# Kernel optimization log

Measured on AMD Instinct MI355X. Metric: run time of the kernel, lower is better.

The kernel has to match this reference:

```python
import jax, jax.numpy as jnp
import numpy as np

D_MODEL = 1024
N_HEADS = 16
D_HEAD = D_MODEL // N_HEADS
D_FF = 4 * D_MODEL
EPS = 1e-5


def _layernorm(x, g, b):
    mu = jnp.mean(x, axis=-1, keepdims=True)
    var = jnp.var(x, axis=-1, keepdims=True)
    return (x - mu) * jax.lax.rsqrt(var + EPS) * g + b


def setup_inputs() -> dict:
    key = jax.random.key(0)
    ks = jax.random.split(key, 16)
    s_attn = 1.0 / np.sqrt(D_MODEL)
    s_ff1 = 1.0 / np.sqrt(D_MODEL)
    s_ff2 = 1.0 / np.sqrt(D_FF)
    inp = {
        'x': jax.random.normal(ks[0], (2, 2048, D_MODEL), dtype=jnp.float32),
        'Wq': jax.random.uniform(ks[1], (D_MODEL, D_MODEL), jnp.float32, -s_attn, s_attn),
        'bq': jax.random.uniform(ks[2], (D_MODEL,), jnp.float32, -s_attn, s_attn),
        'Wk': jax.random.uniform(ks[3], (D_MODEL, D_MODEL), jnp.float32, -s_attn, s_attn),
        'bk': jax.random.uniform(ks[4], (D_MODEL,), jnp.float32, -s_attn, s_attn),
        'Wv': jax.random.uniform(ks[5], (D_MODEL, D_MODEL), jnp.float32, -s_attn, s_attn),
        'bv': jax.random.uniform(ks[6], (D_MODEL,), jnp.float32, -s_attn, s_attn),
        'Wo': jax.random.uniform(ks[7], (D_MODEL, D_MODEL), jnp.float32, -s_attn, s_attn),
        'bo': jax.random.uniform(ks[8], (D_MODEL,), jnp.float32, -s_attn, s_attn),
        'W1': jax.random.uniform(ks[9], (D_MODEL, D_FF), jnp.float32, -s_ff1, s_ff1),
        'b1': jax.random.uniform(ks[10], (D_FF,), jnp.float32, -s_ff1, s_ff1),
        'W2': jax.random.uniform(ks[11], (D_FF, D_MODEL), jnp.float32, -s_ff2, s_ff2),
        'b2': jax.random.uniform(ks[12], (D_MODEL,), jnp.float32, -s_ff2, s_ff2),
        'ln1_g': jnp.ones((D_MODEL,), jnp.float32),
        'ln1_b': jnp.zeros((D_MODEL,), jnp.float32),
        'ln2_g': jnp.ones((D_MODEL,), jnp.float32),
        'ln2_b': jnp.zeros((D_MODEL,), jnp.float32),
    }
    return inp


def reference(x, Wq, bq, Wk, bk, Wv, bv, Wo, bo, W1, b1, W2, b2, ln1_g, ln1_b, ln2_g, ln2_b):
    B, T, D = x.shape
    scale = D_HEAD ** -0.5

    # pre-norm MHSA + residual
    h = _layernorm(x, ln1_g, ln1_b)
    def split(z):  # [B,T,D] -> [B,H,T,d_h]
        return z.reshape(B, T, N_HEADS, D_HEAD).transpose(0, 2, 1, 3)
    Q = split(h @ Wq + bq)
    K = split(h @ Wk + bk)
    V = split(h @ Wv + bv)
    scores = jnp.einsum('bhqd,bhkd->bhqk', Q, K) * scale  # [B,H,T,T]
    attn = jax.nn.softmax(scores, axis=-1)
    out = jnp.einsum('bhqk,bhkd->bhqd', attn, V)
    out = out.transpose(0, 2, 1, 3).reshape(B, T, D)
    x = x + (out @ Wo + bo)

    # pre-norm FFN + residual
    h = _layernorm(x, ln2_g, ln2_b)
    ff = jax.nn.gelu(h @ W1 + b1, approximate=False) @ W2 + b2
    return x + ff
```

## Files before the change

kernel.cpp:

```cpp
#include <hip/hip_runtime.h>
#include <math.h>

#define SEQ   2048
#define DM    1024
#define LDQKV 3072
#define MTOK  4096

typedef float  f32x4   __attribute__((ext_vector_type(4)));
typedef __bf16 bf16x8  __attribute__((ext_vector_type(8)));
typedef short  short8  __attribute__((ext_vector_type(8)));
typedef short  short4v __attribute__((ext_vector_type(4)));

__device__ __forceinline__ short f2bf(float f) {
  union { float f; unsigned u; } v; v.f = f;
  unsigned r = v.u + 0x7fffu + ((v.u >> 16) & 1u);
  return (short)(r >> 16);
}

__device__ __forceinline__ void gl_lds16(const void* g, void* l) {
  __builtin_amdgcn_global_load_lds(
      (const __attribute__((address_space(1))) void*)g,
      (__attribute__((address_space(3))) void*)l, 16, 0, 0);
}

__device__ __forceinline__ f32x4 mfma_bf16(bf16x8 a, bf16x8 b, f32x4 c) {
  return __builtin_amdgcn_mfma_f32_16x16x32_bf16(a, b, c, 0, 0, 0);
}

__device__ __forceinline__ float gelu_f(float x) {
  const float z  = x * 0.70710678118654752f;
  const float az = fabsf(z);
  const float t  = __builtin_amdgcn_rcpf(fmaf(0.3275911f, az, 1.0f));
  float p = fmaf(1.061405429f, t, -1.453152027f);
  p = fmaf(p, t, 1.421413741f);
  p = fmaf(p, t, -0.284496736f);
  p = fmaf(p, t, 0.254829592f);
  p = p * t;
  const float e = __builtin_amdgcn_exp2f(az * az * -1.4426950408889634f);
  float erfp = fmaf(-p, e, 1.0f);
  erfp = (z < 0.f) ? -erfp : erfp;
  return x * fmaf(0.5f, erfp, 0.5f);
}

__global__ __launch_bounds__(256) void transpose_all_k(
    const float* __restrict__ Wq, const float* __restrict__ Wk,
    const float* __restrict__ Wv, const float* __restrict__ Wo,
    const float* __restrict__ W1, const float* __restrict__ W2,
    short* __restrict__ Wqt, short* __restrict__ Wkt, short* __restrict__ Wvt,
    short* __restrict__ Wot, short* __restrict__ W1t, short* __restrict__ W2t)
{
  const int bid = blockIdx.x;
  const float* W; short* Wt; int K, N, nx, ky;
  if (bid < 1024) {
    const int m = bid >> 8, r = bid & 255;
    W  = (m == 0) ? Wq : (m == 1) ? Wk : (m == 2) ? Wv : Wo;
    Wt = (m == 0) ? Wqt : (m == 1) ? Wkt : (m == 2) ? Wvt : Wot;
    K = 1024; N = 1024; nx = r & 15; ky = r >> 4;
  } else if (bid < 2048) {
    const int r = bid - 1024;
    W = W1; Wt = W1t; K = 1024; N = 4096; nx = r & 63; ky = r >> 6;
  } else {
    const int r = bid - 2048;
    W = W2; Wt = W2t; K = 4096; N = 1024; nx = r & 15; ky = r >> 4;
  }
  const int n0 = nx * 64, k0 = ky * 64;

  __shared__ float tile[64][65];
  const int tid = threadIdx.x;
  const int lr = tid >> 4, lc = (tid & 15) * 4;
#pragma unroll
  for (int i = 0; i < 4; i++) {
    const float4 v = *(const float4*)&W[(size_t)(k0 + lr + i * 16) * N + n0 + lc];
    tile[lr + i * 16][lc]     = v.x;
    tile[lr + i * 16][lc + 1] = v.y;
    tile[lr + i * 16][lc + 2] = v.z;
    tile[lr + i * 16][lc + 3] = v.w;
  }
  __syncthreads();
  const int nr = tid >> 3, ks = (tid & 7) * 8;
#pragma unroll
  for (int i = 0; i < 2; i++) {
    short8 o;
#pragma unroll
    for (int j = 0; j < 8; j++) o[j] = f2bf(tile[ks + j][nr + i * 32]);
    *(short8*)&Wt[(size_t)(n0 + nr + i * 32) * K + k0 + ks] = o;
  }
}

__global__ __launch_bounds__(256) void ln_k(
    const float* __restrict__ x, const float* __restrict__ g,
    const float* __restrict__ b, short* __restrict__ out)
{
  const int row = blockIdx.x;
  const int tid = threadIdx.x;
  const float4 v = ((const float4*)(x + (size_t)row * DM))[tid];
  float s  = v.x + v.y + v.z + v.w;
  float ss = v.x * v.x + v.y * v.y + v.z * v.z + v.w * v.w;
#pragma unroll
  for (int m = 32; m >= 1; m >>= 1) { s += __shfl_xor(s, m); ss += __shfl_xor(ss, m); }
  __shared__ float red[8];
  const int wid = tid >> 6;
  if ((tid & 63) == 0) { red[wid] = s; red[4 + wid] = ss; }
  __syncthreads();
  s  = red[0] + red[1] + red[2] + red[3];
  ss = red[4] + red[5] + red[6] + red[7];
  const float mu  = s * (1.f / DM);
  const float var = ss * (1.f / DM) - mu * mu;
  const float rs  = rsqrtf(var + 1e-5f);
  const float4 gv = ((const float4*)g)[tid];
  const float4 bv = ((const float4*)b)[tid];
  short4v o;
  o[0] = f2bf((v.x - mu) * rs * gv.x + bv.x);
  o[1] = f2bf((v.y - mu) * rs * gv.y + bv.y);
  o[2] = f2bf((v.z - mu) * rs * gv.z + bv.z);
  o[3] = f2bf((v.w - mu) * rs * gv.w + bv.w);
  *(short4v*)(out + (size_t)row * DM + tid * 4) = o;
}

__global__ __launch_bounds__(256) void concat_bias_k(
    const float* __restrict__ bq, const float* __restrict__ bk,
    const float* __restrict__ bv, float* __restrict__ o)
{
  int i = blockIdx.x * 256 + threadIdx.x;
  if (i < 3072) {
    float v = (i < 1024) ? bq[i] : (i < 2048 ? bk[i - 1024] : bv[i - 2048]);
    o[i] = v;
  }
}

__global__ __launch_bounds__(256) void vtrans_k(
    const short* __restrict__ V, short* __restrict__ Vt)
{
  const int b = blockIdx.z, h = blockIdx.y, t0 = blockIdx.x * 64;
  __shared__ short tile[64][72];
  const int tid = threadIdx.x;
  const int r = tid >> 2, c = (tid & 3) * 16;
  const short* src = V + (size_t)(b * SEQ + t0 + r) * LDQKV + h * 64 + c;
  *(short8*)&tile[r][c]     = *(const short8*)src;
  *(short8*)&tile[r][c + 8] = *(const short8*)(src + 8);
  __syncthreads();
  const int d = tid >> 2;
  short8 o0, o1;
#pragma unroll
  for (int k = 0; k < 8; k++) o0[k] = tile[c + k][d];
#pragma unroll
  for (int k = 0; k < 8; k++) o1[k] = tile[c + 8 + k][d];
  short* dst = Vt + (((size_t)(b * 16 + h) * 64) + d) * 2048 + t0 + c;
  *(short8*)dst       = o0;
  *(short8*)(dst + 8) = o1;
}

template <bool GELU_, bool RESID, bool OUTBF16>
__global__ __launch_bounds__(512) void gemm256(
    const short* __restrict__ A, const short* __restrict__ Bt,
    const float* __restrict__ bias, const float* __restrict__ resid,
    void* __restrict__ Cout, int M, int N, int K)
{
  __shared__ __align__(16) short Atile[2][256 * 64];
  __shared__ __align__(16) short Btile[2][256 * 64];

  const int tid = threadIdx.x, lane = tid & 63, wid = tid >> 6;
  const int wm = wid >> 2, wn = wid & 3;

  const int nbn = N >> 8;
  const int chunk = gridDim.x >> 3;
  const int swz = (blockIdx.x & 7) * chunk + (blockIdx.x >> 3);
  const int bm = (swz / nbn) * 256;
  const int bn = (swz % nbn) * 256;

  f32x4 acc[8][4] = {};

  const int srow  = wid * 8 + (lane >> 3);
  const int sslot = (lane & 7) ^ ((lane >> 3) & 7);
  const short* Asrc = A  + (size_t)(bm + srow) * K + sslot * 8;
  const short* Bsrc = Bt + (size_t)(bn + srow) * K + sslot * 8;

#define STAGE256(buf, k0)                                                     \
  {                                                                           \
    _Pragma("unroll")                                                         \
    for (int j = 0; j < 4; j++) {                                             \
      gl_lds16(Asrc + (size_t)(j * 64) * K + (k0), &Atile[buf][(j * 64 + wid * 8) * 64]); \
      gl_lds16(Bsrc + (size_t)(j * 64) * K + (k0), &Btile[buf][(j * 64 + wid * 8) * 64]); \
    }                                                                         \
  }

  const int aRowBase = (wm * 128 + (lane & 15)) * 128;
  const int bRowBase = (wn * 64  + (lane & 15)) * 128;
  const int slot0 = (((lane >> 4)    ) ^ (lane & 7)) * 16;
  const int slot1 = (((lane >> 4) + 4) ^ (lane & 7)) * 16;

#define COMPUTE256(buf)                                                       \
  {                                                                           \
    const char* Ab_ = (const char*)&Atile[buf][0];                            \
    const char* Bb_ = (const char*)&Btile[buf][0];                            \
    _Pragma("unroll")                                                         \
    for (int ks = 0; ks < 2; ks++) {                                          \
      const int sl = ks ? slot1 : slot0;                                      \
      bf16x8 a[8], b[4];                                                      \
      _Pragma("unroll")                                                       \
      for (int mi = 0; mi < 8; mi++)                                          \
        a[mi] = *(const bf16x8*)(Ab_ + aRowBase + mi * 2048 + sl);            \
      _Pragma("unroll")                                                       \
      for (int ni = 0; ni < 4; ni++)                                          \
        b[ni] = *(const bf16x8*)(Bb_ + bRowBase + ni * 2048 + sl);            \
      __builtin_amdgcn_s_setprio(1);                                          \
      _Pragma("unroll")                                                       \
      for (int mi = 0; mi < 8; mi++)                                          \
        _Pragma("unroll")                                                     \
        for (int ni = 0; ni < 4; ni++)                                        \
          acc[mi][ni] = mfma_bf16(a[mi], b[ni], acc[mi][ni]);                 \
      __builtin_amdgcn_s_setprio(0);                                          \
    }                                                                         \
  }

  STAGE256(0, 0);
  __syncthreads();

  int cur = 0;
  const int ntiles = K >> 6;
  for (int t = 1; t < ntiles; ++t) {
    STAGE256(cur ^ 1, t * 64);
    COMPUTE256(cur);
    __syncthreads();
    cur ^= 1;
  }
  COMPUTE256(cur);

#pragma unroll
  for (int mi = 0; mi < 8; mi++) {
#pragma unroll
    for (int ni = 0; ni < 4; ni++) {
      const int col = bn + wn * 64 + ni * 16 + (lane & 15);
      const float bs = bias[col];
#pragma unroll
      for (int j = 0; j < 4; j++) {
        const int row = bm + wm * 128 + mi * 16 + (lane >> 4) * 4 + j;
        float v = acc[mi][ni][j] + bs;
        if (GELU_) v = gelu_f(v);
        if (RESID) v += resid[(size_t)row * N + col];
        if (OUTBF16) ((short*)Cout)[(size_t)row * N + col] = f2bf(v);
        else         ((float*)Cout)[(size_t)row * N + col] = v;
      }
    }
  }
#undef STAGE256
#undef COMPUTE256
}

template <bool GELU_, bool RESID, bool OUTBF16>
__global__ __launch_bounds__(512) void gemm256d3(
    const short* __restrict__ A, const short* __restrict__ Bt,
    const float* __restrict__ bias, const float* __restrict__ resid,
    void* __restrict__ Cout, int M, int N, int K)
{
  __shared__ __align__(16) short Ash[4][256 * 32];
  __shared__ __align__(16) short Bsh[4][256 * 32];

  const int tid = threadIdx.x, lane = tid & 63, wid = tid >> 6;
  const int wm = wid >> 2, wn = wid & 3;

  const int nbn = N >> 8;
  const int chunk = gridDim.x >> 3;
  const int swz = (blockIdx.x & 7) * chunk + (blockIdx.x >> 3);
  const int bm = (swz / nbn) * 256;
  const int bn = (swz % nbn) * 256;

  f32x4 acc[8][4] = {};

  const int srow = tid >> 2;
  const int scol = ((tid & 3) ^ ((srow >> 1) & 3)) * 8;
  const short* Asrc = A  + (size_t)(bm + srow) * K + scol;
  const short* Bsrc = Bt + (size_t)(bn + srow) * K + scol;
  const int d0 = (wid * 16) * 32, d1 = (128 + wid * 16) * 32;

#define STAGE_D3(buf, k0)                                                     \
  {                                                                           \
    gl_lds16(Asrc + (k0),                   &Ash[buf][d0]);                   \
    gl_lds16(Asrc + (size_t)128 * K + (k0), &Ash[buf][d1]);                   \
    gl_lds16(Bsrc + (k0),                   &Bsh[buf][d0]);                   \
    gl_lds16(Bsrc + (size_t)128 * K + (k0), &Bsh[buf][d1]);                   \
  }

  const int rslot = ((lane >> 4) ^ ((lane >> 1) & 3)) * 8;
  const int aOff  = (wm * 128 + (lane & 15)) * 32 + rslot;
  const int bOff  = (wn * 64  + (lane & 15)) * 32 + rslot;

#define COMPUTE_D3(buf)                                                       \
  {                                                                           \
    const short* Ab_ = &Ash[buf][0];                                          \
    const short* Bb_ = &Bsh[buf][0];                                          \
    bf16x8 a[8], b[4];                                                        \
    _Pragma("unroll")                                                         \
    for (int mi = 0; mi < 8; mi++)                                            \
      a[mi] = *(const bf16x8*)(Ab_ + aOff + mi * 512);                        \
    _Pragma("unroll")                                                         \
    for (int ni = 0; ni < 4; ni++)                                            \
      b[ni] = *(const bf16x8*)(Bb_ + bOff + ni * 512);                        \
    __builtin_amdgcn_s_setprio(1);                                            \
    _Pragma("unroll")                                                         \
    for (int mi = 0; mi < 8; mi++)                                            \
      _Pragma("unroll")                                                       \
      for (int ni = 0; ni < 4; ni++)                                          \
        acc[mi][ni] = mfma_bf16(a[mi], b[ni], acc[mi][ni]);                   \
    __builtin_amdgcn_s_setprio(0);                                            \
  }

  const int nt = K >> 5;

  STAGE_D3(0, 0);
  STAGE_D3(1, 32);
  STAGE_D3(2, 64);
  asm volatile("s_waitcnt vmcnt(8)" ::: "memory");
  __builtin_amdgcn_s_barrier();
  __builtin_amdgcn_sched_barrier(0);

  for (int t = 0; t < nt; ++t) {
    if (t + 3 < nt) STAGE_D3((t + 3) & 3, (t + 3) * 32);
    COMPUTE_D3(t & 3);
    if (t + 3 < nt)      { asm volatile("s_waitcnt vmcnt(8)" ::: "memory"); }
    else if (t + 2 < nt) { asm volatile("s_waitcnt vmcnt(4)" ::: "memory"); }
    else if (t + 1 < nt) { asm volatile("s_waitcnt vmcnt(0)" ::: "memory"); }
    __builtin_amdgcn_s_barrier();
    __builtin_amdgcn_sched_barrier(0);
  }

#pragma unroll
  for (int mi = 0; mi < 8; mi++) {
#pragma unroll
    for (int ni = 0; ni < 4; ni++) {
      const int col = bn + wn * 64 + ni * 16 + (lane & 15);
      const float bs = bias[col];
#pragma unroll
      for (int j = 0; j < 4; j++) {
        const int row = bm + wm * 128 + mi * 16 + (lane >> 4) * 4 + j;
        float v = acc[mi][ni][j] + bs;
        if (GELU_) v = gelu_f(v);
        if (RESID) v += resid[(size_t)row * N + col];
        if (OUTBF16) ((short*)Cout)[(size_t)row * N + col] = f2bf(v);
        else         ((float*)Cout)[(size_t)row * N + col] = v;
      }
    }
  }
#undef STAGE_D3
#undef COMPUTE_D3
}

template <bool GELU_, bool RESID, bool OUTBF16>
__global__ __launch_bounds__(512) void gemm_bt8(
    const short* __restrict__ A, const short* __restrict__ Bt,
    const float* __restrict__ bias, const float* __restrict__ resid,
    void* __restrict__ Cout, int M, int N, int K)
{
  __shared__ __align__(16) short Ab[2][2][128 * 32];
  __shared__ __align__(16) short Bb[2][2][64 * 32];
  const int tid = threadIdx.x, lane = tid & 63, wid = tid >> 6;
  const int kg = wid >> 2, w2 = wid & 3;
  const int wr = w2 >> 1, wc = w2 & 1;
  const int bm = blockIdx.x * 128, bn = blockIdx.y * 64;

  f32x4 acc[4][2] = {};

  const int r_l = lane >> 2;
  const int c8  = ((lane & 3) ^ ((lane >> 3) & 3)) * 8;
  const short* Ag0 = A  + (size_t)(bm + w2 * 32 + r_l)      * K + c8;
  const short* Ag1 = A  + (size_t)(bm + w2 * 32 + 16 + r_l) * K + c8;
  const short* Bg0 = Bt + (size_t)(bn + w2 * 16 + r_l)      * K + c8;

  const int la0 = (w2 * 32) * 32, la1 = (w2 * 32 + 16) * 32, lb0 = (w2 * 16) * 32;
  const int kbase = kg * 32;
  const int rslot = ((lane >> 4) ^ ((lane >> 1) & 3)) * 8;

  gl_lds16(Ag0 + kbase, &Ab[kg][0][la0]);
  gl_lds16(Ag1 + kbase, &Ab[kg][0][la1]);
  gl_lds16(Bg0 + kbase, &Bb[kg][0][lb0]);
  __syncthreads();

  const int nsteps = K >> 6;
  int cur = 0;
  for (int i = 1; i < nsteps; ++i) {
    const int k0 = i * 64 + kbase;
    const int nxt = cur ^ 1;
    gl_lds16(Ag0 + k0, &Ab[kg][nxt][la0]);
    gl_lds16(Ag1 + k0, &Ab[kg][nxt][la1]);
    gl_lds16(Bg0 + k0, &Bb[kg][nxt][lb0]);

    bf16x8 a[4], b[2];
#pragma unroll
    for (int mi = 0; mi < 4; mi++)
      a[mi] = *(const bf16x8*)&Ab[kg][cur][(wr * 64 + mi * 16 + (lane & 15)) * 32 + rslot];
#pragma unroll
    for (int ni = 0; ni < 2; ni++)
      b[ni] = *(const bf16x8*)&Bb[kg][cur][(wc * 32 + ni * 16 + (lane & 15)) * 32 + rslot];
#pragma unroll
    for (int mi = 0; mi < 4; mi++)
#pragma unroll
      for (int ni = 0; ni < 2; ni++)
        acc[mi][ni] = mfma_bf16(a[mi], b[ni], acc[mi][ni]);

    __syncthreads();
    cur = nxt;
  }

  {
    bf16x8 a[4], b[2];
#pragma unroll
    for (int mi = 0; mi < 4; mi++)
      a[mi] = *(const bf16x8*)&Ab[kg][cur][(wr * 64 + mi * 16 + (lane & 15)) * 32 + rslot];
#pragma unroll
    for (int ni = 0; ni < 2; ni++)
      b[ni] = *(const bf16x8*)&Bb[kg][cur][(wc * 32 + ni * 16 + (lane & 15)) * 32 + rslot];
#pragma unroll
    for (int mi = 0; mi < 4; mi++)
#pragma unroll
      for (int ni = 0; ni < 2; ni++)
        acc[mi][ni] = mfma_bf16(a[mi], b[ni], acc[mi][ni]);
  }

  __syncthreads();

  float* red = (float*)&Ab[0][0][0];
  const int lslot = w2 * 64 + lane;
  if (kg == 1) {
    *(f32x4*)&red[((0 * 256) + lslot) * 4]        = acc[0][0];
    *(f32x4*)&red[((1 * 256) + lslot) * 4]        = acc[0][1];
    *(f32x4*)&red[((2 * 256) + lslot) * 4]        = acc[1][0];
    *(f32x4*)&red[((3 * 256) + lslot) * 4]        = acc[1][1];
  } else {
    *(f32x4*)&red[((1024 + 0 * 256) + lslot) * 4] = acc[2][0];
    *(f32x4*)&red[((1024 + 1 * 256) + lslot) * 4] = acc[2][1];
    *(f32x4*)&red[((1024 + 2 * 256) + lslot) * 4] = acc[3][0];
    *(f32x4*)&red[((1024 + 3 * 256) + lslot) * 4] = acc[3][1];
  }
  __syncthreads();

#define BT8_STORE(MI, NI)                                                     \
  {                                                                           \
    const int col = bn + wc * 32 + (NI) * 16 + (lane & 15);                   \
    const float bs = bias[col];                                               \
    _Pragma("unroll")                                                         \
    for (int j = 0; j < 4; j++) {                                             \
      const int row = bm + wr * 64 + (MI) * 16 + (lane >> 4) * 4 + j;         \
      float v = acc[MI][NI][j] + bs;                                          \
      if (GELU_) v = gelu_f(v);                                               \
      if (RESID) v += resid[(size_t)row * N + col];                           \
      if (OUTBF16) ((short*)Cout)[(size_t)row * N + col] = f2bf(v);           \
      else         ((float*)Cout)[(size_t)row * N + col] = v;                 \
    }                                                                         \
  }

  if (kg == 0) {
    acc[0][0] += *(const f32x4*)&red[((0 * 256) + lslot) * 4];
    acc[0][1] += *(const f32x4*)&red[((1 * 256) + lslot) * 4];
    acc[1][0] += *(const f32x4*)&red[((2 * 256) + lslot) * 4];
    acc[1][1] += *(const f32x4*)&red[((3 * 256) + lslot) * 4];
    BT8_STORE(0, 0); BT8_STORE(0, 1); BT8_STORE(1, 0); BT8_STORE(1, 1);
  } else {
    acc[2][0] += *(const f32x4*)&red[((1024 + 0 * 256) + lslot) * 4];
    acc[2][1] += *(const f32x4*)&red[((1024 + 1 * 256) + lslot) * 4];
    acc[3][0] += *(const f32x4*)&red[((1024 + 2 * 256) + lslot) * 4];
    acc[3][1] += *(const f32x4*)&red[((1024 + 3 * 256) + lslot) * 4];
    BT8_STORE(2, 0); BT8_STORE(2, 1); BT8_STORE(3, 0); BT8_STORE(3, 1);
  }
#undef BT8_STORE
}

__global__ __launch_bounds__(512, 4) void attn_k(
    const short* __restrict__ Qg, const short* __restrict__ Kg,
    const short* __restrict__ Vt, short* __restrict__ Og)
{
  const int phys = blockIdx.x;
  const int lg = (phys & 7) * 64 + (phys >> 3);
  const int q0 = (lg & 15) * 128;
  const int h  = (lg >> 4) & 15;
  const int b  = lg >> 8;

  const int tid = threadIdx.x, lane = tid & 63, w = tid >> 6;
  const int qlane = lane & 15, g = lane >> 4;

  __shared__ __align__(16) short Kl[2][128 * 64];
  __shared__ __align__(16) short Vl[2][64 * 128];

  const size_t qrow = (size_t)(b * SEQ + q0 + w * 16 + qlane) * LDQKV + h * 64;
  const bf16x8 qf0 = *(const bf16x8*)&Qg[qrow + g * 8];
  const bf16x8 qf1 = *(const bf16x8*)&Qg[qrow + 32 + g * 8];

  const int kslot = (lane & 7) ^ ((lane >> 3) & 7);
  const short* Kg_a[2];
#pragma unroll
  for (int i = 0; i < 2; i++) {
    const int r  = i * 64 + w * 8 + (lane >> 3);
    const int kc = r >> 4, gr = (r >> 2) & 3, jr = r & 3;
    const int a  = 32 * (kc & 3) + 8 * gr + 4 * (kc >> 2) + jr;
    Kg_a[i] = Kg + ((size_t)(b * SEQ) + a) * LDQKV + h * 64 + kslot * 8;
  }
  const short* Vg_s[2];
#pragma unroll
  for (int i = 0; i < 2; i++) {
    const int d  = i * 32 + w * 4 + (lane >> 4);
    const int vs = (lane & 15) ^ (d & 15);
    Vg_s[i] = Vt + ((size_t)(b * 16 + h) * 64 + d) * 2048 + vs * 8;
  }

  float m_run = -1e30f, l_run = 0.f;
  f32x4 oacc[4] = {};
  const float C = 0.125f * 1.44269504088896f;

#pragma unroll
  for (int i = 0; i < 2; i++) {
    gl_lds16(Kg_a[i], &Kl[0][(i * 64 + w * 8) * 64]);
    gl_lds16(Vg_s[i], &Vl[0][(i * 32 + w * 4) * 128]);
  }
  __syncthreads();

  int cur = 0;
  for (int kt = 0; kt < SEQ; kt += 128) {
    const int nxt = cur ^ 1;
    if (kt + 128 < SEQ) {
#pragma unroll
      for (int i = 0; i < 2; i++) {
        gl_lds16(Kg_a[i] + (size_t)(kt + 128) * LDQKV, &Kl[nxt][(i * 64 + w * 8) * 64]);
        gl_lds16(Vg_s[i] + (kt + 128),                 &Vl[nxt][(i * 32 + w * 4) * 128]);
      }
    }
    const char* KbC = (const char*)&Kl[cur][0];
    const char* VbC = (const char*)&Vl[cur][0];

    f32x4 s[8];
#pragma unroll
    for (int kc = 0; kc < 8; kc++) {
      const int kr = kc * 16 + qlane;
      const char* kp = KbC + kr * 128;
      const int sw = (kr & 7) << 4;
      bf16x8 kf0 = *(const bf16x8*)(kp + ((g * 16) ^ sw));
      bf16x8 kf1 = *(const bf16x8*)(kp + ((64 + g * 16) ^ sw));
      f32x4 z = {};
      z = mfma_bf16(kf0, qf0, z);
      z = mfma_bf16(kf1, qf1, z);
      s[kc] = z;
    }

    f32x4 m4 = s[0];
#pragma unroll
    for (int kc = 1; kc < 8; kc++) {
      m4[0] = fmaxf(m4[0], s[kc][0]); m4[1] = fmaxf(m4[1], s[kc][1]);
      m4[2] = fmaxf(m4[2], s[kc][2]); m4[3] = fmaxf(m4[3], s[kc][3]);
    }
    float mt = fmaxf(fmaxf(m4[0], m4[1]), fmaxf(m4[2], m4[3]));
    mt = fmaxf(mt, __shfl_xor(mt, 16));
    mt = fmaxf(mt, __shfl_xor(mt, 32));

    if (!__all(mt - m_run <= 40.0f)) {
      const float mnew = fmaxf(m_run, mt);
      const float r = __builtin_amdgcn_exp2f((m_run - mnew) * C);
      m_run = mnew;
      l_run *= r;
#pragma unroll
      for (int j = 0; j < 4; j++) {
        const float rj = __shfl(r, g * 4 + j);
#pragma unroll
        for (int dt = 0; dt < 4; dt++) oacc[dt][j] *= rj;
      }
    }

    const float nmc = -m_run * C;
    float rs = 0.f;
    unsigned pw[4][4];
#pragma unroll
    for (int kc = 0; kc < 8; kc++) {
      f32x4 p;
#pragma unroll
      for (int j = 0; j < 4; j++) p[j] = __builtin_amdgcn_exp2f(fmaf(s[kc][j], C, nmc));
      rs += (p[0] + p[1]) + (p[2] + p[3]);
      unsigned w0, w1;
      asm("v_cvt_pk_bf16_f32 %0, %1, %2" : "=v"(w0) : "v"(p[0]), "v"(p[1]));
      asm("v_cvt_pk_bf16_f32 %0, %1, %2" : "=v"(w1) : "v"(p[2]), "v"(p[3]));
      pw[kc & 3][2 * (kc >> 2) + 0] = w0;
      pw[kc & 3][2 * (kc >> 2) + 1] = w1;
    }
    rs += __shfl_xor(rs, 16);
    rs += __shfl_xor(rs, 32);
    l_run += rs;

#pragma unroll
    for (int ks = 0; ks < 4; ks++) {
      union { unsigned u[4]; bf16x8 v; } pf;
      pf.u[0] = pw[ks][0]; pf.u[1] = pw[ks][1];
      pf.u[2] = pw[ks][2]; pf.u[3] = pw[ks][3];
#pragma unroll
      for (int dt = 0; dt < 4; dt++) {
        const int vr = dt * 16 + qlane;
        bf16x8 vf = *(const bf16x8*)(VbC + vr * 256 + ((64 * ks + 16 * g) ^ ((vr & 15) << 4)));
        oacc[dt] = mfma_bf16(pf.v, vf, oacc[dt]);
      }
    }

    __syncthreads();
    cur = nxt;
  }

  const float linv = 1.f / l_run;
#pragma unroll
  for (int j = 0; j < 4; j++) {
    const float lj = __shfl(linv, g * 4 + j);
    const int tok = q0 + w * 16 + g * 4 + j;
#pragma unroll
    for (int dt = 0; dt < 4; dt++)
      Og[(size_t)(b * SEQ + tok) * DM + h * 64 + dt * 16 + qlane] = f2bf(oacc[dt][j] * lj);
  }
}

extern "C" void kernel_launch(void* const* d_in, const int* in_sizes, int n_in,
                              void* d_out, int out_size, void* d_ws, size_t ws_size,
                              hipStream_t stream)
{
  const float* x    = (const float*)d_in[0];
  const float* Wq   = (const float*)d_in[1];
  const float* bq   = (const float*)d_in[2];
  const float* Wk   = (const float*)d_in[3];
  const float* bk   = (const float*)d_in[4];
  const float* Wv   = (const float*)d_in[5];
  const float* bv   = (const float*)d_in[6];
  const float* Wo   = (const float*)d_in[7];
  const float* bo   = (const float*)d_in[8];
  const float* W1   = (const float*)d_in[9];
  const float* b1   = (const float*)d_in[10];
  const float* W2   = (const float*)d_in[11];
  const float* b2   = (const float*)d_in[12];
  const float* ln1g = (const float*)d_in[13];
  const float* ln1b = (const float*)d_in[14];
  const float* ln2g = (const float*)d_in[15];
  const float* ln2b = (const float*)d_in[16];

  char* ws = (char*)d_ws;
  const size_t MB = 1024 * 1024;
  short* Wqkvt = (short*)(ws + 0 * MB);
  short* Wqt   = Wqkvt;
  short* Wkt   = (short*)(ws + 2 * MB);
  short* Wvt   = (short*)(ws + 4 * MB);
  short* Wot   = (short*)(ws + 6 * MB);
  short* W1t   = (short*)(ws + 8 * MB);
  short* W2t   = (short*)(ws + 16 * MB);
  short* hbuf  = (short*)(ws + 24 * MB);
  short* QKV   = (short*)(ws + 32 * MB);
  short* AO    = (short*)(ws + 56 * MB);
  float* x1    = (float*)(ws + 64 * MB);
  short* Vtb   = (short*)(ws + 64 * MB);
  float* bqkv  = (float*)(ws + 80 * MB);
  short* gbuf  = (short*)(ws + 32 * MB);

  dim3 tb(256);

  transpose_all_k<<<dim3(3072), tb, 0, stream>>>(
      Wq, Wk, Wv, Wo, W1, W2, Wqt, Wkt, Wvt, Wot, W1t, W2t);
  concat_bias_k<<<dim3(12), tb, 0, stream>>>(bq, bk, bv, bqkv);

  ln_k<<<dim3(MTOK), tb, 0, stream>>>(x, ln1g, ln1b, hbuf);

  gemm256<false, false, true><<<dim3(192), dim3(512), 0, stream>>>(
      hbuf, Wqkvt, bqkv, nullptr, QKV, MTOK, 3072, 1024);

  vtrans_k<<<dim3(32, 16, 2), tb, 0, stream>>>(QKV + 2048, Vtb);

  attn_k<<<dim3(512), dim3(512), 0, stream>>>(QKV, QKV + 1024, Vtb, AO);

  gemm_bt8<false, true, false><<<dim3(32, 16), dim3(512), 0, stream>>>(
      AO, Wot, bo, x, x1, MTOK, 1024, 1024);

  ln_k<<<dim3(MTOK), tb, 0, stream>>>(x1, ln2g, ln2b, hbuf);

  gemm256d3<true, false, true><<<dim3(256), dim3(512), 0, stream>>>(
      hbuf, W1t, b1, nullptr, gbuf, MTOK, 4096, 1024);

  gemm_bt8<false, true, false><<<dim3(32, 16), dim3(512), 0, stream>>>(
      gbuf, W2t, b2, x1, (float*)d_out, MTOK, 1024, 4096);
}
```

Baseline: 243.8 us.

## Replace split-K 128x64 GEMM with 128x128 tile, 4-stage LDS pipeline

```diff
diff --git a/kernel.cpp b/kernel.cpp
--- a/kernel.cpp
+++ b/kernel.cpp
@@ -346,122 +346,105 @@
 }
 
 template <bool GELU_, bool RESID, bool OUTBF16>
-__global__ __launch_bounds__(512) void gemm_bt8(
+__global__ __launch_bounds__(512) void gemm128d3(
     const short* __restrict__ A, const short* __restrict__ Bt,
     const float* __restrict__ bias, const float* __restrict__ resid,
     void* __restrict__ Cout, int M, int N, int K)
 {
-  __shared__ __align__(16) short Ab[2][2][128 * 32];
-  __shared__ __align__(16) short Bb[2][2][64 * 32];
+  __shared__ __align__(16) short Ash[4][128 * 64];
+  __shared__ __align__(16) short Bsh[4][128 * 64];
+
   const int tid = threadIdx.x, lane = tid & 63, wid = tid >> 6;
-  const int kg = wid >> 2, w2 = wid & 3;
-  const int wr = w2 >> 1, wc = w2 & 1;
-  const int bm = blockIdx.x * 128, bn = blockIdx.y * 64;
+  const int wm = wid >> 2, wn = wid & 3;
+
+  const int nbn = N >> 7;
+  const int chunk = gridDim.x >> 3;
+  const int swz = (blockIdx.x & 7) * chunk + (blockIdx.x >> 3);
+  const int bm = (swz / nbn) * 128;
+  const int bn = (swz % nbn) * 128;
 
   f32x4 acc[4][2] = {};
 
-  const int r_l = lane >> 2;
-  const int c8  = ((lane & 3) ^ ((lane >> 3) & 3)) * 8;
-  const short* Ag0 = A  + (size_t)(bm + w2 * 32 + r_l)      * K + c8;
-  const short* Ag1 = A  + (size_t)(bm + w2 * 32 + 16 + r_l) * K + c8;
-  const short* Bg0 = Bt + (size_t)(bn + w2 * 16 + r_l)      * K + c8;
-
-  const int la0 = (w2 * 32) * 32, la1 = (w2 * 32 + 16) * 32, lb0 = (w2 * 16) * 32;
-  const int kbase = kg * 32;
-  const int rslot = ((lane >> 4) ^ ((lane >> 1) & 3)) * 8;
-
-  gl_lds16(Ag0 + kbase, &Ab[kg][0][la0]);
-  gl_lds16(Ag1 + kbase, &Ab[kg][0][la1]);
-  gl_lds16(Bg0 + kbase, &Bb[kg][0][lb0]);
-  __syncthreads();
-
-  const int nsteps = K >> 6;
-  int cur = 0;
-  for (int i = 1; i < nsteps; ++i) {
-    const int k0 = i * 64 + kbase;
-    const int nxt = cur ^ 1;
-    gl_lds16(Ag0 + k0, &Ab[kg][nxt][la0]);
-    gl_lds16(Ag1 + k0, &Ab[kg][nxt][la1]);
-    gl_lds16(Bg0 + k0, &Bb[kg][nxt][lb0]);
-
-    bf16x8 a[4], b[2];
-#pragma unroll
-    for (int mi = 0; mi < 4; mi++)
-      a[mi] = *(const bf16x8*)&Ab[kg][cur][(wr * 64 + mi * 16 + (lane & 15)) * 32 + rslot];
-#pragma unroll
-    for (int ni = 0; ni < 2; ni++)
-      b[ni] = *(const bf16x8*)&Bb[kg][cur][(wc * 32 + ni * 16 + (lane & 15)) * 32 + rslot];
-#pragma unroll
-    for (int mi = 0; mi < 4; mi++)
-#pragma unroll
-      for (int ni = 0; ni < 2; ni++)
-        acc[mi][ni] = mfma_bf16(a[mi], b[ni], acc[mi][ni]);
-
-    __syncthreads();
-    cur = nxt;
-  }
-
-  {
-    bf16x8 a[4], b[2];
-#pragma unroll
-    for (int mi = 0; mi < 4; mi++)
-      a[mi] = *(const bf16x8*)&Ab[kg][cur][(wr * 64 + mi * 16 + (lane & 15)) * 32 + rslot];
-#pragma unroll
-    for (int ni = 0; ni < 2; ni++)
-      b[ni] = *(const bf16x8*)&Bb[kg][cur][(wc * 32 + ni * 16 + (lane & 15)) * 32 + rslot];
-#pragma unroll
-    for (int mi = 0; mi < 4; mi++)
-#pragma unroll
-      for (int ni = 0; ni < 2; ni++)
-        acc[mi][ni] = mfma_bf16(a[mi], b[ni], acc[mi][ni]);
-  }
-
-  __syncthreads();
-
-  float* red = (float*)&Ab[0][0][0];
-  const int lslot = w2 * 64 + lane;
-  if (kg == 1) {
-    *(f32x4*)&red[((0 * 256) + lslot) * 4]        = acc[0][0];
-    *(f32x4*)&red[((1 * 256) + lslot) * 4]        = acc[0][1];
-    *(f32x4*)&red[((2 * 256) + lslot) * 4]        = acc[1][0];
-    *(f32x4*)&red[((3 * 256) + lslot) * 4]        = acc[1][1];
-  } else {
-    *(f32x4*)&red[((1024 + 0 * 256) + lslot) * 4] = acc[2][0];
-    *(f32x4*)&red[((1024 + 1 * 256) + lslot) * 4] = acc[2][1];
-    *(f32x4*)&red[((1024 + 2 * 256) + lslot) * 4] = acc[3][0];
-    *(f32x4*)&red[((1024 + 3 * 256) + lslot) * 4] = acc[3][1];
-  }
-  __syncthreads();
-
-#define BT8_STORE(MI, NI)                                                     \
+  const int srow  = wid * 8 + (lane >> 3);
+  const int sslot = (lane & 7) ^ ((lane >> 3) & 7);
+  const short* Asrc = A  + (size_t)(bm + srow) * K + sslot * 8;
+  const short* Bsrc = Bt + (size_t)(bn + srow) * K + sslot * 8;
+
+#define STAGE_128(buf, k0)                                                    \
   {                                                                           \
-    const int col = bn + wc * 32 + (NI) * 16 + (lane & 15);                   \
-    const float bs = bias[col];                                               \
+    gl_lds16(Asrc + (k0),                  &Ash[buf][(wid * 8) * 64]);        \
+    gl_lds16(Asrc + (size_t)64 * K + (k0), &Ash[buf][(64 + wid * 8) * 64]);   \
+    gl_lds16(Bsrc + (k0),                  &Bsh[buf][(wid * 8) * 64]);        \
+    gl_lds16(Bsrc + (size_t)64 * K + (k0), &Bsh[buf][(64 + wid * 8) * 64]);   \
+  }
+
+  const int aRowBase = (wm * 64 + (lane & 15)) * 128;
+  const int bRowBase = (wn * 32 + (lane & 15)) * 128;
+  const int slot0 = (((lane >> 4)    ) ^ (lane & 7)) * 16;
+  const int slot1 = (((lane >> 4) + 4) ^ (lane & 7)) * 16;
+
+#define COMPUTE_128(buf)                                                      \
+  {                                                                           \
+    const char* Ab_ = (const char*)&Ash[buf][0];                              \
+    const char* Bb_ = (const char*)&Bsh[buf][0];                              \
     _Pragma("unroll")                                                         \
-    for (int j = 0; j < 4; j++) {                                             \
-      const int row = bm + wr * 64 + (MI) * 16 + (lane >> 4) * 4 + j;         \
-      float v = acc[MI][NI][j] + bs;                                          \
-      if (GELU_) v = gelu_f(v);                                               \
-      if (RESID) v += resid[(size_t)row * N + col];                           \
-      if (OUTBF16) ((short*)Cout)[(size_t)row * N + col] = f2bf(v);           \
-      else         ((float*)Cout)[(size_t)row * N + col] = v;                 \
+    for (int ks = 0; ks < 2; ks++) {                                          \
+      const int sl = ks ? slot1 : slot0;                                      \
+      bf16x8 a[4], b[2];                                                      \
+      _Pragma("unroll")                                                       \
+      for (int mi = 0; mi < 4; mi++)                                          \
+        a[mi] = *(const bf16x8*)(Ab_ + aRowBase + mi * 2048 + sl);            \
+      _Pragma("unroll")                                                       \
+      for (int ni = 0; ni < 2; ni++)                                          \
+        b[ni] = *(const bf16x8*)(Bb_ + bRowBase + ni * 2048 + sl);            \
+      __builtin_amdgcn_s_setprio(1);                                          \
+      _Pragma("unroll")                                                       \
+      for (int mi = 0; mi < 4; mi++)                                          \
+        _Pragma("unroll")                                                     \
+        for (int ni = 0; ni < 2; ni++)                                        \
+          acc[mi][ni] = mfma_bf16(a[mi], b[ni], acc[mi][ni]);                 \
+      __builtin_amdgcn_s_setprio(0);                                          \
     }                                                                         \
   }
 
-  if (kg == 0) {
-    acc[0][0] += *(const f32x4*)&red[((0 * 256) + lslot) * 4];
-    acc[0][1] += *(const f32x4*)&red[((1 * 256) + lslot) * 4];
-    acc[1][0] += *(const f32x4*)&red[((2 * 256) + lslot) * 4];
-    acc[1][1] += *(const f32x4*)&red[((3 * 256) + lslot) * 4];
-    BT8_STORE(0, 0); BT8_STORE(0, 1); BT8_STORE(1, 0); BT8_STORE(1, 1);
-  } else {
-    acc[2][0] += *(const f32x4*)&red[((1024 + 0 * 256) + lslot) * 4];
-    acc[2][1] += *(const f32x4*)&red[((1024 + 1 * 256) + lslot) * 4];
-    acc[3][0] += *(const f32x4*)&red[((1024 + 2 * 256) + lslot) * 4];
-    acc[3][1] += *(const f32x4*)&red[((1024 + 3 * 256) + lslot) * 4];
-    BT8_STORE(2, 0); BT8_STORE(2, 1); BT8_STORE(3, 0); BT8_STORE(3, 1);
-  }
-#undef BT8_STORE
+  const int nt = K >> 6;
+
+  STAGE_128(0, 0);
+  STAGE_128(1, 64);
+  STAGE_128(2, 128);
+  asm volatile("s_waitcnt vmcnt(8)" ::: "memory");
+  __builtin_amdgcn_s_barrier();
+  __builtin_amdgcn_sched_barrier(0);
+
+  for (int t = 0; t < nt; ++t) {
+    if (t + 3 < nt) STAGE_128((t + 3) & 3, (t + 3) * 64);
+    COMPUTE_128(t & 3);
+    if (t + 3 < nt)      { asm volatile("s_waitcnt vmcnt(8)" ::: "memory"); }
+    else if (t + 2 < nt) { asm volatile("s_waitcnt vmcnt(4)" ::: "memory"); }
+    else if (t + 1 < nt) { asm volatile("s_waitcnt vmcnt(0)" ::: "memory"); }
+    __builtin_amdgcn_s_barrier();
+    __builtin_amdgcn_sched_barrier(0);
+  }
+
+#pragma unroll
+  for (int mi = 0; mi < 4; mi++) {
+#pragma unroll
+    for (int ni = 0; ni < 2; ni++) {
+      const int col = bn + wn * 32 + ni * 16 + (lane & 15);
+      const float bs = bias[col];
+#pragma unroll
+      for (int j = 0; j < 4; j++) {
+        const int row = bm + wm * 64 + mi * 16 + (lane >> 4) * 4 + j;
+        float v = acc[mi][ni][j] + bs;
+        if (GELU_) v = gelu_f(v);
+        if (RESID) v += resid[(size_t)row * N + col];
+        if (OUTBF16) ((short*)Cout)[(size_t)row * N + col] = f2bf(v);
+        else         ((float*)Cout)[(size_t)row * N + col] = v;
+      }
+    }
+  }
+#undef STAGE_128
+#undef COMPUTE_128
 }
 
 __global__ __launch_bounds__(512, 4) void attn_k(
@@ -663,7 +646,7 @@
 
   attn_k<<<dim3(512), dim3(512), 0, stream>>>(QKV, QKV + 1024, Vtb, AO);
 
-  gemm_bt8<false, true, false><<<dim3(32, 16), dim3(512), 0, stream>>>(
+  gemm128d3<false, true, false><<<dim3(256), dim3(512), 0, stream>>>(
       AO, Wot, bo, x, x1, MTOK, 1024, 1024);
 
   ln_k<<<dim3(MTOK), tb, 0, stream>>>(x1, ln2g, ln2b, hbuf);
@@ -671,6 +654,6 @@
   gemm256d3<true, false, true><<<dim3(256), dim3(512), 0, stream>>>(
       hbuf, W1t, b1, nullptr, gbuf, MTOK, 4096, 1024);
 
-  gemm_bt8<false, true, false><<<dim3(32, 16), dim3(512), 0, stream>>>(
+  gemm128d3<false, true, false><<<dim3(256), dim3(512), 0, stream>>>(
       gbuf, W2t, b2, x1, (float*)d_out, MTOK, 1024, 4096);
 }
```

New measurement: 256.9 us. +5.4%, slower.
